# Kernel tuning notes

Measured on AMD Instinct MI355X. Metric: run time of the kernel, lower is better.

The kernel has to match this reference:

```python
import jax, jax.numpy as jnp
import numpy as np

PARENTS = np.array([-1, 0, 1, 1, 1])
NECK_CHAIN = np.array([1, 0])  # neck joint (1) up to root (0)
B, V, F, J, S, E = 512, 5023, 9976, 5, 100, 50
L_STAT, L_DYN, L_FULL, N_BUCKET = 51, 17, 68, 79


def rodrigues(rvec):
    """Axis-angle [N,3] -> rotation matrices [N,3,3]."""
    angle = jnp.linalg.norm(rvec + 1e-8, axis=-1, keepdims=True)  # [N,1]
    axis = rvec / angle
    s = jnp.sin(angle)[..., None]
    c = jnp.cos(angle)[..., None]
    rx, ry, rz = axis[:, 0], axis[:, 1], axis[:, 2]
    z = jnp.zeros_like(rx)
    K = jnp.stack([z, -rz, ry, rz, z, -rx, -ry, rx, z], axis=-1).reshape(-1, 3, 3)
    I = jnp.eye(3, dtype=rvec.dtype)
    return I + s * K + (1.0 - c) * (K @ K)


def verts2lmk(vertices, faces, lmk_faces_idx, lmk_bary):
    lmk_faces = faces[lmk_faces_idx]                               # [B,L,3]
    lmk_verts = jax.vmap(lambda v, f: v[f])(vertices, lmk_faces)   # [B,L,3verts,3xyz]
    return jnp.einsum('blfc,blf->blc', lmk_verts, lmk_bary)


def setup_inputs() -> dict:
    key = jax.random.key(0)
    ks = jax.random.split(key, 16)
    shape_params = jax.random.normal(ks[0], (B, S), jnp.float32)
    expression_params = jax.random.normal(ks[1], (B, E), jnp.float32)
    pose_params = 0.2 * jax.random.normal(ks[2], (B, 6), jnp.float32)
    eye_pose_params = 0.1 * jax.random.normal(ks[3], (B, 6), jnp.float32)
    v_template = jax.random.normal(ks[4], (V, 3), jnp.float32) * 0.1
    shapedirs = jax.random.normal(ks[5], (V, 3, S + E), jnp.float32) * 0.01
    posedirs = jax.random.normal(ks[6], ((J - 1) * 9, V * 3), jnp.float32) * 0.01
    jr = jax.random.uniform(ks[7], (J, V), jnp.float32)
    J_regressor = jr / jnp.sum(jr, axis=1, keepdims=True)
    lbs_weights = jax.nn.softmax(jax.random.normal(ks[8], (V, J), jnp.float32), axis=-1)
    faces = jax.random.randint(ks[9], (F, 3), 0, V)
    lmk_faces_idx = jax.random.randint(ks[10], (L_STAT,), 0, F)
    lb = jax.random.uniform(ks[11], (L_STAT, 3), jnp.float32) + 1e-3
    lmk_bary_coords = lb / jnp.sum(lb, axis=-1, keepdims=True)
    dynamic_lmk_faces_idx = jax.random.randint(ks[12], (N_BUCKET, L_DYN), 0, F)
    db = jax.random.uniform(ks[13], (N_BUCKET, L_DYN, 3), jnp.float32) + 1e-3
    dynamic_lmk_bary_coords = db / jnp.sum(db, axis=-1, keepdims=True)
    full_lmk_faces_idx = jax.random.randint(ks[14], (L_FULL,), 0, F)
    fb = jax.random.uniform(ks[15], (L_FULL, 3), jnp.float32) + 1e-3
    full_lmk_bary_coords = fb / jnp.sum(fb, axis=-1, keepdims=True)
    return {
        'shape_params': shape_params, 'expression_params': expression_params,
        'pose_params': pose_params, 'eye_pose_params': eye_pose_params,
        'v_template': v_template, 'shapedirs': shapedirs, 'posedirs': posedirs,
        'J_regressor': J_regressor, 'lbs_weights': lbs_weights, 'faces': faces,
        'lmk_faces_idx': lmk_faces_idx, 'lmk_bary_coords': lmk_bary_coords,
        'dynamic_lmk_faces_idx': dynamic_lmk_faces_idx,
        'dynamic_lmk_bary_coords': dynamic_lmk_bary_coords,
        'full_lmk_faces_idx': full_lmk_faces_idx,
        'full_lmk_bary_coords': full_lmk_bary_coords,
    }


def reference(shape_params, expression_params, pose_params, eye_pose_params,
              v_template, shapedirs, posedirs, J_regressor, lbs_weights, faces,
              lmk_faces_idx, lmk_bary_coords, dynamic_lmk_faces_idx,
              dynamic_lmk_bary_coords, full_lmk_faces_idx, full_lmk_bary_coords):
    b = shape_params.shape[0]
    nv = v_template.shape[0]
    dt = shape_params.dtype
    betas = jnp.concatenate([shape_params, expression_params], axis=1)          # [B,150]
    neck = jnp.zeros((b, 3), dtype=dt)
    full_pose = jnp.concatenate(
        [pose_params[:, :3], neck, pose_params[:, 3:], eye_pose_params], axis=1)  # [B,15]
    # shape + expression blendshapes
    v_shaped = v_template[None] + jnp.einsum('bl,vcl->bvc', betas, shapedirs)   # [B,V,3]
    joints = jnp.einsum('jv,bvc->bjc', J_regressor, v_shaped)                   # [B,5,3]
    rot_mats = rodrigues(full_pose.reshape(-1, 3)).reshape(b, J, 3, 3)          # [B,5,3,3]
    I3 = jnp.eye(3, dtype=dt)
    pose_feature = (rot_mats[:, 1:] - I3).reshape(b, -1)                        # [B,36]
    v_posed = v_shaped + (pose_feature @ posedirs).reshape(b, nv, 3)
    # kinematic chain -> global joint transforms
    rel_J = joints.at[:, 1:].add(-joints[:, PARENTS[1:]])
    tm = jnp.zeros((b, J, 4, 4), dtype=dt)
    tm = tm.at[:, :, :3, :3].set(rot_mats).at[:, :, :3, 3].set(rel_J).at[:, :, 3, 3].set(1.0)
    chain = [tm[:, 0]]
    for i in range(1, J):
        chain.append(chain[PARENTS[i]] @ tm[:, i])
    A = jnp.stack(chain, axis=1)                                                # [B,5,4,4]
    Rj = jnp.einsum('bjmn,bjn->bjm', A[:, :, :3, :3], joints)
    A_rel = A.at[:, :, :3, 3].add(-Rj)
    # per-vertex skinning
    T = jnp.einsum('vj,bjmn->bvmn', lbs_weights, A_rel)                         # [B,V,4,4]
    vertices = jnp.einsum('bvmn,bvn->bvm', T[:, :, :3, :3], v_posed) + T[:, :, :3, 3]
    # dynamic contour landmark selection from neck kin-chain relative rotation
    aa = full_pose.reshape(b, J, 3)[:, NECK_CHAIN]                              # [B,2,3]
    rc = rodrigues(aa.reshape(-1, 3)).reshape(b, len(NECK_CHAIN), 3, 3)
    rel_rot = jnp.broadcast_to(I3, (b, 3, 3))
    for idx in range(len(NECK_CHAIN)):
        rel_rot = rc[:, idx] @ rel_rot
    sy = jnp.sqrt(rel_rot[:, 0, 0] ** 2 + rel_rot[:, 1, 0] ** 2)
    y_deg = jnp.arctan2(-rel_rot[:, 2, 0], sy) * (180.0 / np.pi)
    y_rot = jnp.round(jnp.minimum(y_deg, 39.0)).astype(jnp.int32)
    neg_mask = y_rot < 0
    big_neg = y_rot < -39
    neg_vals = jnp.where(big_neg, 78, 39 - y_rot)
    y_rot = jnp.where(neg_mask, neg_vals, y_rot)                                # [B] in [0,79)
    dyn_faces = dynamic_lmk_faces_idx[y_rot]                                    # [B,17]
    dyn_bary = dynamic_lmk_bary_coords[y_rot]                                   # [B,17,3]
    lf = jnp.concatenate([dyn_faces, jnp.broadcast_to(lmk_faces_idx[None], (b, lmk_faces_idx.shape[0]))], axis=1)
    lb = jnp.concatenate([dyn_bary, jnp.broadcast_to(lmk_bary_coords[None], (b,) + lmk_bary_coords.shape)], axis=1)
    landmarks2d = verts2lmk(vertices, faces, lf, lb)
    ff = jnp.broadcast_to(full_lmk_faces_idx[None], (b, full_lmk_faces_idx.shape[0]))
    fb = jnp.broadcast_to(full_lmk_bary_coords[None], (b,) + full_lmk_bary_coords.shape)
    landmarks3d = verts2lmk(vertices, faces, ff, fb)
    return (vertices, landmarks2d, landmarks3d)
```

## Files before the change

### kernel.cpp

```cpp
#include <hip/hip_runtime.h>
#include <cstddef>
#include <cstdint>

#define cB   512
#define cV   5023
#define cS   100
#define cE   50
#define cJ   5
#define cLD  17
#define cLF  68

#define cV3    15069
#define cNPAD  15072

#define OUT_V  ((size_t)cB * cV * 3)
#define OUT_L  ((size_t)cB * cLF * 3)

#define WS_BTN    ((size_t)0)
#define WS_ATM    (WS_BTN + (size_t)cNPAD * 96)
#define WS_JS2    (WS_ATM + (size_t)cB * 96)
#define WS_AREL   (WS_JS2 + 2432)
#define WS_YROT   (WS_AREL + (size_t)cB * 60)
#define WS_JSPART (WS_YROT + 512)

typedef __attribute__((ext_vector_type(8))) short short8;
typedef __attribute__((ext_vector_type(4))) float f32x4;

__device__ __forceinline__ unsigned short f2bf(float x) {
  unsigned int u = __float_as_uint(x);
  u = (u + 0x7fffu + ((u >> 16) & 1u)) >> 16;
  return (unsigned short)u;
}

__device__ __forceinline__ void rodrigues9(float rx, float ry, float rz, float* R) {
  float a0 = rx + 1e-8f, a1 = ry + 1e-8f, a2 = rz + 1e-8f;
  float angle = sqrtf(a0 * a0 + a1 * a1 + a2 * a2);
  float inv = 1.0f / angle;
  float x = rx * inv, y = ry * inv, z = rz * inv;
  float s = sinf(angle), c = cosf(angle);
  float t = 1.0f - c;
  float xy = x * y, xz = x * z, yz = y * z;
  R[0] = 1.0f - t * (y * y + z * z);
  R[1] = -s * z + t * xy;
  R[2] =  s * y + t * xz;
  R[3] =  s * z + t * xy;
  R[4] = 1.0f - t * (x * x + z * z);
  R[5] = -s * x + t * yz;
  R[6] = -s * y + t * xz;
  R[7] =  s * x + t * yz;
  R[8] = 1.0f - t * (x * x + y * y);
}

__global__ __launch_bounds__(512) void k_dirs(
    const float* __restrict__ sd, const float* __restrict__ pd,
    const float* __restrict__ jreg, const float* __restrict__ vt,
    unsigned int* __restrict__ btn_u, float* __restrict__ JSpart) {
  __shared__ float sdt[96 * 152];
  __shared__ unsigned short pdt[96 * 38];
  const int t = threadIdx.x;
  const int nb = blockIdx.x;
  const int n0 = nb * 96, v0 = nb * 32;

  const size_t gbase = (size_t)n0 * 150;
  for (int idx = t; idx < 14400; idx += 512) {
    size_t g = gbase + idx;
    float v = (g < (size_t)cV3 * 150) ? sd[g] : 0.f;
    int row = idx / 150, col = idx - row * 150;
    sdt[row * 152 + col] = v;
  }
  for (int e = t; e < 3456; e += 512) {
    int pdk = e / 96, row = e - pdk * 96;
    int n = n0 + row;
    float v = (n < cV3) ? pd[(size_t)pdk * cV3 + n] : 0.f;
    pdt[row * 38 + pdk] = f2bf(v);
  }
  __syncthreads();

#pragma unroll
  for (int it = 0; it < 18; ++it) {
    int e = t + it * 512;
    int row = e / 96, d = e - row * 96;
    unsigned int wv;
    if (d < 75) {
      wv = (unsigned int)f2bf(sdt[row * 152 + 2 * d]) |
           ((unsigned int)f2bf(sdt[row * 152 + 2 * d + 1]) << 16);
    } else if (d < 93) {
      wv = (unsigned int)pdt[row * 38 + (d - 75) * 2] |
           ((unsigned int)pdt[row * 38 + (d - 75) * 2 + 1] << 16);
    } else {
      wv = 0u;
    }
    btn_u[(size_t)(n0 + row) * 96 + d] = wv;
  }

  if (t < 453) {
    int c = t / 151, l = t - c * 151;
    float acc[5] = {0.f, 0.f, 0.f, 0.f, 0.f};
#pragma unroll 8
    for (int v_loc = 0; v_loc < 32; ++v_loc) {
      int v = v0 + v_loc;
      bool ok = (v < cV);
      float x = (l < 150) ? sdt[(v_loc * 3 + c) * 152 + l]
                          : (ok ? vt[v * 3 + c] : 0.f);
#pragma unroll
      for (int j = 0; j < 5; ++j) {
        float g = ok ? jreg[j * cV + v] : 0.f;
        acc[j] = fmaf(g, x, acc[j]);
      }
    }
#pragma unroll
    for (int j = 0; j < 5; ++j)
      JSpart[(size_t)nb * 2272 + (j * 3 + c) * 151 + l] = acc[j];
  }
}

__global__ void k_jsred(const float* __restrict__ JSpart, float* __restrict__ JS2) {
  int e = blockIdx.x * 256 + threadIdx.x;
  if (e >= 2265) return;
  float s = 0.f;
#pragma unroll 8
  for (int p = 0; p < 157; ++p)
    s += JSpart[(size_t)p * 2272 + e];
  int jc = e / 151, l = e - jc * 151;
  JS2[l * 16 + jc] = s;
}

__global__ __launch_bounds__(256) void k_batch(
    const float* __restrict__ shp, const float* __restrict__ expr,
    const float* __restrict__ pose, const float* __restrict__ eyep,
    const float* __restrict__ JS2g, float* __restrict__ Arel,
    int* __restrict__ yrot, unsigned int* __restrict__ atm_u) {
  __shared__ float js2[151 * 16];
  __shared__ float sb[32 * 153];
  __shared__ float pfs[32 * 36];
  const int t = threadIdx.x;
  const int b0 = blockIdx.x * 32;
  for (int i = t; i < 151 * 16; i += 256) js2[i] = JS2g[i];
  for (int e = t; e < 3200; e += 256) {
    int bl = e / 100, l = e - bl * 100;
    sb[bl * 153 + l] = shp[(size_t)(b0 + bl) * 100 + l];
  }
  for (int e = t; e < 1600; e += 256) {
    int bl = e / 50, l = e - bl * 50;
    sb[bl * 153 + 100 + l] = expr[(size_t)(b0 + bl) * 50 + l];
  }
  __syncthreads();

  if (t < 32) {
    int b = b0 + t;
    float jnt[5][3];
    {
      const f32x4* J4 = (const f32x4*)(js2 + 150 * 16);
      f32x4 A = J4[0], Bq = J4[1], Cq = J4[2], Dq = J4[3];
      jnt[0][0] = A.x;  jnt[0][1] = A.y;  jnt[0][2] = A.z;
      jnt[1][0] = A.w;  jnt[1][1] = Bq.x; jnt[1][2] = Bq.y;
      jnt[2][0] = Bq.z; jnt[2][1] = Bq.w; jnt[2][2] = Cq.x;
      jnt[3][0] = Cq.y; jnt[3][1] = Cq.z; jnt[3][2] = Cq.w;
      jnt[4][0] = Dq.x; jnt[4][1] = Dq.y; jnt[4][2] = Dq.z;
    }
    for (int l = 0; l < 150; ++l) {
      const f32x4* J4 = (const f32x4*)(js2 + l * 16);
      f32x4 A = J4[0], Bq = J4[1], Cq = J4[2], Dq = J4[3];
      float beta = sb[t * 153 + l];
      jnt[0][0] = fmaf(beta, A.x,  jnt[0][0]);
      jnt[0][1] = fmaf(beta, A.y,  jnt[0][1]);
      jnt[0][2] = fmaf(beta, A.z,  jnt[0][2]);
      jnt[1][0] = fmaf(beta, A.w,  jnt[1][0]);
      jnt[1][1] = fmaf(beta, Bq.x, jnt[1][1]);
      jnt[1][2] = fmaf(beta, Bq.y, jnt[1][2]);
      jnt[2][0] = fmaf(beta, Bq.z, jnt[2][0]);
      jnt[2][1] = fmaf(beta, Bq.w, jnt[2][1]);
      jnt[2][2] = fmaf(beta, Cq.x, jnt[2][2]);
      jnt[3][0] = fmaf(beta, Cq.y, jnt[3][0]);
      jnt[3][1] = fmaf(beta, Cq.z, jnt[3][1]);
      jnt[3][2] = fmaf(beta, Cq.w, jnt[3][2]);
      jnt[4][0] = fmaf(beta, Dq.x, jnt[4][0]);
      jnt[4][1] = fmaf(beta, Dq.y, jnt[4][1]);
      jnt[4][2] = fmaf(beta, Dq.z, jnt[4][2]);
    }
    float fp[5][3];
    fp[0][0] = pose[b * 6 + 0]; fp[0][1] = pose[b * 6 + 1]; fp[0][2] = pose[b * 6 + 2];
    fp[1][0] = 0.f; fp[1][1] = 0.f; fp[1][2] = 0.f;
    fp[2][0] = pose[b * 6 + 3]; fp[2][1] = pose[b * 6 + 4]; fp[2][2] = pose[b * 6 + 5];
    fp[3][0] = eyep[b * 6 + 0]; fp[3][1] = eyep[b * 6 + 1]; fp[3][2] = eyep[b * 6 + 2];
    fp[4][0] = eyep[b * 6 + 3]; fp[4][1] = eyep[b * 6 + 4]; fp[4][2] = eyep[b * 6 + 5];
    float R[5][9];
#pragma unroll
    for (int j = 0; j < 5; ++j) rodrigues9(fp[j][0], fp[j][1], fp[j][2], R[j]);
#pragma unroll
    for (int j = 1; j < 5; ++j)
#pragma unroll
      for (int r = 0; r < 9; ++r) {
        float id = (r == 0 || r == 4 || r == 8) ? 1.f : 0.f;
        pfs[t * 36 + (j - 1) * 9 + r] = R[j][r] - id;
      }
    float rel[5][3];
#pragma unroll
    for (int c = 0; c < 3; ++c) {
      rel[0][c] = jnt[0][c];
      rel[1][c] = jnt[1][c] - jnt[0][c];
      rel[2][c] = jnt[2][c] - jnt[1][c];
      rel[3][c] = jnt[3][c] - jnt[1][c];
      rel[4][c] = jnt[4][c] - jnt[1][c];
    }
    float GR[5][9], Gt[5][3];
#pragma unroll
    for (int r = 0; r < 9; ++r) GR[0][r] = R[0][r];
#pragma unroll
    for (int c = 0; c < 3; ++c) Gt[0][c] = rel[0][c];
    const int par[5] = {0, 0, 1, 1, 1};
#pragma unroll
    for (int j = 1; j < 5; ++j) {
      int p = par[j];
#pragma unroll
      for (int r = 0; r < 3; ++r) {
#pragma unroll
        for (int cc = 0; cc < 3; ++cc)
          GR[j][r * 3 + cc] = GR[p][r * 3 + 0] * R[j][0 + cc] +
                              GR[p][r * 3 + 1] * R[j][3 + cc] +
                              GR[p][r * 3 + 2] * R[j][6 + cc];
        Gt[j][r] = Gt[p][r] + GR[p][r * 3 + 0] * rel[j][0] +
                              GR[p][r * 3 + 1] * rel[j][1] +
                              GR[p][r * 3 + 2] * rel[j][2];
      }
    }
#pragma unroll
    for (int j = 0; j < 5; ++j)
#pragma unroll
      for (int r = 0; r < 3; ++r) {
        float tj = Gt[j][r] - (GR[j][r * 3 + 0] * jnt[j][0] +
                               GR[j][r * 3 + 1] * jnt[j][1] +
                               GR[j][r * 3 + 2] * jnt[j][2]);
        Arel[b * 60 + j * 12 + r * 4 + 0] = GR[j][r * 3 + 0];
        Arel[b * 60 + j * 12 + r * 4 + 1] = GR[j][r * 3 + 1];
        Arel[b * 60 + j * 12 + r * 4 + 2] = GR[j][r * 3 + 2];
        Arel[b * 60 + j * 12 + r * 4 + 3] = tj;
      }
    float Ra[9], Rb[9];
    rodrigues9(fp[1][0], fp[1][1], fp[1][2], Ra);
    rodrigues9(fp[0][0], fp[0][1], fp[0][2], Rb);
    float r00 = Rb[0] * Ra[0] + Rb[1] * Ra[3] + Rb[2] * Ra[6];
    float r10 = Rb[3] * Ra[0] + Rb[4] * Ra[3] + Rb[5] * Ra[6];
    float r20 = Rb[6] * Ra[0] + Rb[7] * Ra[3] + Rb[8] * Ra[6];
    float sy = sqrtf(r00 * r00 + r10 * r10);
    float ydeg = atan2f(-r20, sy) * 57.29577951308232f;
    int y = (int)rintf(fminf(ydeg, 39.0f));
    if (y < 0) y = (y < -39) ? 78 : (39 - y);
    yrot[b] = y;
  }
  __syncthreads();

#pragma unroll
  for (int it = 0; it < 12; ++it) {
    int e = t + it * 256;
    int bl = e / 96, d = e - bl * 96;
    unsigned int wv;
    if (d < 75) {
      wv = (unsigned int)f2bf(sb[bl * 153 + 2 * d]) |
           ((unsigned int)f2bf(sb[bl * 153 + 2 * d + 1]) << 16);
    } else if (d < 93) {
      wv = (unsigned int)f2bf(pfs[bl * 36 + (d - 75) * 2]) |
           ((unsigned int)f2bf(pfs[bl * 36 + (d - 75) * 2 + 1]) << 16);
    } else {
      wv = 0u;
    }
    atm_u[(size_t)(b0 + bl) * 96 + d] = wv;
  }
}

__global__ __launch_bounds__(256) void k_main(
    const unsigned short* __restrict__ BTn, const unsigned short* __restrict__ ATm,
    const float* __restrict__ Arel, const float* __restrict__ vtempl,
    const float* __restrict__ lbw, float* __restrict__ out) {
  __shared__ __align__(16) unsigned short smem[19200];
  float* Pf = (float*)smem;

  const int bid = blockIdx.x;
  const int r8 = bid & 7, q = bid >> 3;
  const int mb = q & 7, nbh = q >> 3;
  const int nb = (nbh << 3) | r8;
  if (nb >= 157) return;

  const int t = threadIdx.x;
  const int w = t >> 6, L = t & 63;
  const int wm = w >> 1, wn = w & 1;
  const int lr = L & 15, lq = L >> 4;

  const unsigned short* bsrc = BTn + (size_t)nb * 96 * 192;
  uint4 bst[9];
#pragma unroll
  for (int it = 0; it < 9; ++it)
    bst[it] = *(const uint4*)(bsrc + ((size_t)(t + it * 256)) * 8);
#pragma unroll
  for (int it = 0; it < 9; ++it) {
    int e = t + it * 256;
    int row = e / 24, col = e - row * 24;
    *(uint4*)(smem + row * 200 + col * 8) = bst[it];
  }
  __syncthreads();

  f32x4 acc[2][3];
#pragma unroll
  for (int mt = 0; mt < 2; ++mt)
#pragma unroll
    for (int nt = 0; nt < 3; ++nt) acc[mt][nt] = (f32x4){0.f, 0.f, 0.f, 0.f};

  const unsigned short* abase = ATm + ((size_t)mb * 64 + wm * 32 + lr) * 192 + lq * 8;
  short8 af0 = *(const short8*)(abase);
  short8 af1 = *(const short8*)(abase + 16 * 192);
#pragma unroll
  for (int ks = 0; ks < 6; ++ks) {
    short8 nf0, nf1;
    if (ks < 5) {
      nf0 = *(const short8*)(abase + (ks + 1) * 32);
      nf1 = *(const short8*)(abase + 16 * 192 + (ks + 1) * 32);
    }
    const int ko = ks * 32 + lq * 8;
    short8 bf[3];
#pragma unroll
    for (int nt = 0; nt < 3; ++nt)
      bf[nt] = *(const short8*)(smem + (wn * 48 + nt * 16 + lr) * 200 + ko);
#pragma unroll
    for (int nt = 0; nt < 3; ++nt) {
      acc[0][nt] = __builtin_amdgcn_mfma_f32_16x16x32_bf16(af0, bf[nt], acc[0][nt], 0, 0, 0);
      acc[1][nt] = __builtin_amdgcn_mfma_f32_16x16x32_bf16(af1, bf[nt], acc[1][nt], 0, 0, 0);
    }
    af0 = nf0; af1 = nf1;
  }
  __syncthreads();

#pragma unroll
  for (int mt = 0; mt < 2; ++mt)
#pragma unroll
    for (int nt = 0; nt < 3; ++nt) {
      int m_base = wm * 32 + mt * 16 + lq * 4;
      int n_loc  = wn * 48 + nt * 16 + lr;
      *(f32x4*)(Pf + n_loc * 68 + m_base) = acc[mt][nt];
    }
  __syncthreads();

  const int v_loc = t & 31, bgrp = t >> 5;
  const int v = nb * 32 + v_loc;
  float wj[5], vtl[3];
  const bool vok = (v < cV);
#pragma unroll
  for (int j = 0; j < 5; ++j) wj[j] = vok ? lbw[v * 5 + j] : 0.f;
#pragma unroll
  for (int c = 0; c < 3; ++c) vtl[c] = vok ? vtempl[v * 3 + c] : 0.f;

#pragma unroll
  for (int i = 0; i < 8; ++i) {
    const int b_loc = bgrp * 8 + i;
    const float* qb = Arel + ((size_t)mb * 64 + b_loc) * 60;
    float px = Pf[(v_loc * 3 + 0) * 68 + b_loc] + vtl[0];
    float py = Pf[(v_loc * 3 + 1) * 68 + b_loc] + vtl[1];
    float pz = Pf[(v_loc * 3 + 2) * 68 + b_loc] + vtl[2];
    float o0 = 0.f, o1 = 0.f, o2 = 0.f;
#pragma unroll
    for (int j = 0; j < 5; ++j) {
      f32x4 q0 = *(const f32x4*)(qb + j * 12);
      f32x4 q1 = *(const f32x4*)(qb + j * 12 + 4);
      f32x4 q2 = *(const f32x4*)(qb + j * 12 + 8);
      float s0 = q0.x * px + q0.y * py + q0.z * pz + q0.w;
      float s1 = q1.x * px + q1.y * py + q1.z * pz + q1.w;
      float s2 = q2.x * px + q2.y * py + q2.z * pz + q2.w;
      o0 = fmaf(wj[j], s0, o0);
      o1 = fmaf(wj[j], s1, o1);
      o2 = fmaf(wj[j], s2, o2);
    }
    if (vok) {
      const int b = mb * 64 + b_loc;
      size_t off = ((size_t)b * cV + v) * 3;
      out[off + 0] = o0;
      out[off + 1] = o1;
      out[off + 2] = o2;
    }
  }
}

__global__ void k_lmk(const float* __restrict__ verts, const int* __restrict__ faces,
                      const int* __restrict__ lmkf, const float* __restrict__ lmkb,
                      const int* __restrict__ dynf, const float* __restrict__ dynb,
                      const int* __restrict__ fullf, const float* __restrict__ fullb,
                      const int* __restrict__ yrot, float* __restrict__ out) {
  int id = blockIdx.x * 256 + threadIdx.x;
  if (id >= cB * cLF * 2) return;
  int sel = id & 1;
  int r = id >> 1;
  int b = r / cLF, l = r - b * cLF;
  const float* vb = verts + (size_t)b * cV * 3;
  int f; float w0, w1, w2; size_t o;
  if (sel == 0) {
    if (l < cLD) {
      int yb = yrot[b];
      f = dynf[yb * cLD + l];
      const float* bp = dynb + ((size_t)yb * cLD + l) * 3;
      w0 = bp[0]; w1 = bp[1]; w2 = bp[2];
    } else {
      f = lmkf[l - cLD];
      const float* bp = lmkb + (size_t)(l - cLD) * 3;
      w0 = bp[0]; w1 = bp[1]; w2 = bp[2];
    }
    o = OUT_V + ((size_t)b * cLF + l) * 3;
  } else {
    f = fullf[l];
    const float* bp = fullb + (size_t)l * 3;
    w0 = bp[0]; w1 = bp[1]; w2 = bp[2];
    o = OUT_V + OUT_L + ((size_t)b * cLF + l) * 3;
  }
  int i0 = faces[f * 3 + 0] * 3, i1 = faces[f * 3 + 1] * 3, i2 = faces[f * 3 + 2] * 3;
  out[o + 0] = w0 * vb[i0 + 0] + w1 * vb[i1 + 0] + w2 * vb[i2 + 0];
  out[o + 1] = w0 * vb[i0 + 1] + w1 * vb[i1 + 1] + w2 * vb[i2 + 1];
  out[o + 2] = w0 * vb[i0 + 2] + w1 * vb[i1 + 2] + w2 * vb[i2 + 2];
}

extern "C" void kernel_launch(void* const* d_in, const int* in_sizes, int n_in,
                              void* d_out, int out_size, void* d_ws, size_t ws_size,
                              hipStream_t stream) {
  (void)in_sizes; (void)n_in; (void)out_size; (void)ws_size;
  const float* shp  = (const float*)d_in[0];
  const float* expr = (const float*)d_in[1];
  const float* pose = (const float*)d_in[2];
  const float* eyep = (const float*)d_in[3];
  const float* vt   = (const float*)d_in[4];
  const float* sd   = (const float*)d_in[5];
  const float* pd   = (const float*)d_in[6];
  const float* jreg = (const float*)d_in[7];
  const float* lbw  = (const float*)d_in[8];
  const int*   fcs  = (const int*)d_in[9];
  const int*   lmkf = (const int*)d_in[10];
  const float* lmkb = (const float*)d_in[11];
  const int*   dynf = (const int*)d_in[12];
  const float* dynb = (const float*)d_in[13];
  const int*   fullf= (const int*)d_in[14];
  const float* fullb= (const float*)d_in[15];
  float* out = (float*)d_out;
  float* ws  = (float*)d_ws;

  unsigned short* BTn = (unsigned short*)(ws + WS_BTN);
  unsigned short* ATm = (unsigned short*)(ws + WS_ATM);
  float* JS2    = ws + WS_JS2;
  float* Arel   = ws + WS_AREL;
  int*   yrot   = (int*)(ws + WS_YROT);
  float* JSpart = ws + WS_JSPART;

  k_dirs<<<157, 512, 0, stream>>>(sd, pd, jreg, vt, (unsigned int*)BTn, JSpart);
  k_jsred<<<9, 256, 0, stream>>>(JSpart, JS2);
  k_batch<<<16, 256, 0, stream>>>(shp, expr, pose, eyep, JS2, Arel, yrot,
                                  (unsigned int*)ATm);
  k_main<<<1280, 256, 0, stream>>>(BTn, ATm, Arel, vt, lbw, out);
  k_lmk<<<272, 256, 0, stream>>>(out, fcs, lmkf, lmkb, dynf, dynb, fullf, fullb, yrot, out);
}
```

Baseline: 195.1 us.

## Convert shapedirs to bf16 inside main GEMM and split preprocessing across more blocks

Drops the precomputed bf16 B-matrix workspace. The main kernel now reads fp32 shapedirs directly and converts them to bf16 into shared memory, and only a small transposed posedirs bf16 buffer is prebuilt. The joint-regression partial sums are spread over 628 small blocks plus separate posedirs-transpose blocks, and the reduction uses 8 partial groups per element with a shared-memory tree. This removes a 157-block preprocessing pass and the write and re-read of the B workspace. In exchange, each of the 8 batch-tile blocks that share an N tile re-reads fp32 shapedirs and repeats the conversion, which is more global traffic inside k_main.

```diff
diff --git a/kernel.cpp b/kernel.cpp
--- a/kernel.cpp
+++ b/kernel.cpp
@@ -16,11 +16,11 @@
 #define OUT_V  ((size_t)cB * cV * 3)
 #define OUT_L  ((size_t)cB * cLF * 3)
 
-#define WS_BTN    ((size_t)0)
-#define WS_ATM    (WS_BTN + (size_t)cNPAD * 96)
-#define WS_JS2    (WS_ATM + (size_t)cB * 96)
+#define WS_PDT    ((size_t)0)
+#define WS_ATM    (WS_PDT + 271296)
+#define WS_JS2    (WS_ATM + 49152)
 #define WS_AREL   (WS_JS2 + 2432)
-#define WS_YROT   (WS_AREL + (size_t)cB * 60)
+#define WS_YROT   (WS_AREL + 30720)
 #define WS_JSPART (WS_YROT + 512)
 
 typedef __attribute__((ext_vector_type(8))) short short8;
@@ -51,78 +51,79 @@
   R[8] = 1.0f - t * (x * x + y * y);
 }
 
-__global__ __launch_bounds__(512) void k_dirs(
+__global__ __launch_bounds__(512) void k_aux(
     const float* __restrict__ sd, const float* __restrict__ pd,
     const float* __restrict__ jreg, const float* __restrict__ vt,
-    unsigned int* __restrict__ btn_u, float* __restrict__ JSpart) {
-  __shared__ float sdt[96 * 152];
-  __shared__ unsigned short pdt[96 * 38];
+    unsigned int* __restrict__ pdt16_u, float* __restrict__ JSpart) {
+  __shared__ unsigned short T[2304];
   const int t = threadIdx.x;
-  const int nb = blockIdx.x;
-  const int n0 = nb * 96, v0 = nb * 32;
-
-  const size_t gbase = (size_t)n0 * 150;
-  for (int idx = t; idx < 14400; idx += 512) {
-    size_t g = gbase + idx;
-    float v = (g < (size_t)cV3 * 150) ? sd[g] : 0.f;
-    int row = idx / 150, col = idx - row * 150;
-    sdt[row * 152 + col] = v;
-  }
-  for (int e = t; e < 3456; e += 512) {
-    int pdk = e / 96, row = e - pdk * 96;
-    int n = n0 + row;
-    float v = (n < cV3) ? pd[(size_t)pdk * cV3 + n] : 0.f;
-    pdt[row * 38 + pdk] = f2bf(v);
-  }
-  __syncthreads();
-
-#pragma unroll
-  for (int it = 0; it < 18; ++it) {
-    int e = t + it * 512;
-    int row = e / 96, d = e - row * 96;
-    unsigned int wv;
-    if (d < 75) {
-      wv = (unsigned int)f2bf(sdt[row * 152 + 2 * d]) |
-           ((unsigned int)f2bf(sdt[row * 152 + 2 * d + 1]) << 16);
-    } else if (d < 93) {
-      wv = (unsigned int)pdt[row * 38 + (d - 75) * 2] |
-           ((unsigned int)pdt[row * 38 + (d - 75) * 2 + 1] << 16);
-    } else {
-      wv = 0u;
-    }
-    btn_u[(size_t)(n0 + row) * 96 + d] = wv;
-  }
-
-  if (t < 453) {
+  const int bid = blockIdx.x;
+  if (bid < 628) {
+    if (t >= 453) return;
     int c = t / 151, l = t - c * 151;
+    int v0 = bid * 8;
     float acc[5] = {0.f, 0.f, 0.f, 0.f, 0.f};
+#pragma unroll
+    for (int vi = 0; vi < 8; ++vi) {
+      int v = v0 + vi;
+      bool ok = (v < cV);
+      int vc = ok ? v : 0;
+      float x;
+      if (l < 150) x = ok ? sd[(size_t)(v * 3 + c) * 150 + l] : 0.f;
+      else         x = ok ? vt[v * 3 + c] : 0.f;
+#pragma unroll
+      for (int j = 0; j < 5; ++j)
+        acc[j] = fmaf(jreg[j * cV + vc], x, acc[j]);
+    }
+#pragma unroll
+    for (int j = 0; j < 5; ++j)
+      JSpart[(size_t)bid * 2272 + (j * 3 + c) * 151 + l] = acc[j];
+  } else {
+    const int n0 = (bid - 628) * 64;
+    for (int e = t; e < 2304; e += 512) {
+      int kk = e >> 6, ln = e & 63;
+      int n = n0 + ln;
+      float v = (n < cV3) ? pd[(size_t)kk * cV3 + n] : 0.f;
+      T[ln * 36 + kk] = f2bf(v);
+    }
+    __syncthreads();
+    for (int e = t; e < 1152; e += 512) {
+      int ln = e / 18, d = e - ln * 18;
+      int n = n0 + ln;
+      if (n < cNPAD) {
+        unsigned int wv = (unsigned int)T[ln * 36 + 2 * d] |
+                          ((unsigned int)T[ln * 36 + 2 * d + 1] << 16);
+        pdt16_u[(size_t)n * 18 + d] = wv;
+      }
+    }
+  }
+}
+
+__global__ __launch_bounds__(256) void k_jsred(const float* __restrict__ JSpart,
+                                               float* __restrict__ JS2) {
+  __shared__ float red[256];
+  const int t = threadIdx.x;
+  const int e = blockIdx.x * 32 + (t & 31);
+  const int pg = t >> 5;
+  float s = 0.f;
+  if (e < 2265) {
 #pragma unroll 8
-    for (int v_loc = 0; v_loc < 32; ++v_loc) {
-      int v = v0 + v_loc;
-      bool ok = (v < cV);
-      float x = (l < 150) ? sdt[(v_loc * 3 + c) * 152 + l]
-                          : (ok ? vt[v * 3 + c] : 0.f);
-#pragma unroll
-      for (int j = 0; j < 5; ++j) {
-        float g = ok ? jreg[j * cV + v] : 0.f;
-        acc[j] = fmaf(g, x, acc[j]);
-      }
-    }
-#pragma unroll
-    for (int j = 0; j < 5; ++j)
-      JSpart[(size_t)nb * 2272 + (j * 3 + c) * 151 + l] = acc[j];
-  }
-}
-
-__global__ void k_jsred(const float* __restrict__ JSpart, float* __restrict__ JS2) {
-  int e = blockIdx.x * 256 + threadIdx.x;
-  if (e >= 2265) return;
-  float s = 0.f;
-#pragma unroll 8
-  for (int p = 0; p < 157; ++p)
-    s += JSpart[(size_t)p * 2272 + e];
-  int jc = e / 151, l = e - jc * 151;
-  JS2[l * 16 + jc] = s;
+    for (int p = pg; p < 628; p += 8)
+      s += JSpart[(size_t)p * 2272 + e];
+  }
+  red[t] = s;
+  __syncthreads();
+  if (t < 128) red[t] += red[t + 128];
+  __syncthreads();
+  if (t < 64) red[t] += red[t + 64];
+  __syncthreads();
+  if (t < 32) {
+    float v = red[t] + red[t + 32];
+    if (e < 2265) {
+      int jc = e / 151, l = e - jc * 151;
+      JS2[l * 16 + jc] = v;
+    }
+  }
 }
 
 __global__ __launch_bounds__(256) void k_batch(
@@ -269,9 +270,10 @@
 }
 
 __global__ __launch_bounds__(256) void k_main(
-    const unsigned short* __restrict__ BTn, const unsigned short* __restrict__ ATm,
-    const float* __restrict__ Arel, const float* __restrict__ vtempl,
-    const float* __restrict__ lbw, float* __restrict__ out) {
+    const float* __restrict__ sd, const unsigned int* __restrict__ pdt16_u,
+    const unsigned short* __restrict__ ATm, const float* __restrict__ Arel,
+    const float* __restrict__ vtempl, const float* __restrict__ lbw,
+    float* __restrict__ out) {
   __shared__ __align__(16) unsigned short smem[19200];
   float* Pf = (float*)smem;
 
@@ -282,22 +284,50 @@
   if (nb >= 157) return;
 
   const int t = threadIdx.x;
+  const int n0 = nb * 96;
+
+  {
+    const float* sbase = sd + (size_t)n0 * 150;
+    const int vrows = (cV3 - n0 < 96) ? (cV3 - n0) : 96;
+    const int vunits = vrows * 75;
+#pragma unroll
+    for (int it = 0; it < 29; ++it) {
+      int u = t + it * 256;
+      if (u < 7200) {
+        float fx = 0.f, fy = 0.f;
+        if (u < vunits) {
+          float2 f2 = *(const float2*)(sbase + 2 * (size_t)u);
+          fx = f2.x; fy = f2.y;
+        }
+        unsigned int wv = (unsigned int)f2bf(fx) | ((unsigned int)f2bf(fy) << 16);
+        int row = u / 75, cp = u - row * 75;
+        *(unsigned int*)((char*)smem + row * 400 + cp * 4) = wv;
+      }
+    }
+    const unsigned int* pdu = pdt16_u + (size_t)n0 * 18;
+#pragma unroll
+    for (int it = 0; it < 7; ++it) {
+      int u = t + it * 256;
+      if (u < 1728) {
+        unsigned int wv = pdu[u];
+        int row = u / 18, d = u - row * 18;
+        *(unsigned int*)((char*)smem + row * 400 + 300 + d * 4) = wv;
+      }
+    }
+#pragma unroll
+    for (int it = 0; it < 3; ++it) {
+      int u = t + it * 256;
+      if (u < 672) {
+        int row = u / 7, d = u - row * 7;
+        *(unsigned int*)((char*)smem + row * 400 + 372 + d * 4) = 0u;
+      }
+    }
+  }
+  __syncthreads();
+
   const int w = t >> 6, L = t & 63;
   const int wm = w >> 1, wn = w & 1;
   const int lr = L & 15, lq = L >> 4;
-
-  const unsigned short* bsrc = BTn + (size_t)nb * 96 * 192;
-  uint4 bst[9];
-#pragma unroll
-  for (int it = 0; it < 9; ++it)
-    bst[it] = *(const uint4*)(bsrc + ((size_t)(t + it * 256)) * 8);
-#pragma unroll
-  for (int it = 0; it < 9; ++it) {
-    int e = t + it * 256;
-    int row = e / 24, col = e - row * 24;
-    *(uint4*)(smem + row * 200 + col * 8) = bst[it];
-  }
-  __syncthreads();
 
   f32x4 acc[2][3];
 #pragma unroll
@@ -437,17 +467,17 @@
   float* out = (float*)d_out;
   float* ws  = (float*)d_ws;
 
-  unsigned short* BTn = (unsigned short*)(ws + WS_BTN);
-  unsigned short* ATm = (unsigned short*)(ws + WS_ATM);
+  unsigned int*   pdt16 = (unsigned int*)(ws + WS_PDT);
+  unsigned short* ATm   = (unsigned short*)(ws + WS_ATM);
   float* JS2    = ws + WS_JS2;
   float* Arel   = ws + WS_AREL;
   int*   yrot   = (int*)(ws + WS_YROT);
   float* JSpart = ws + WS_JSPART;
 
-  k_dirs<<<157, 512, 0, stream>>>(sd, pd, jreg, vt, (unsigned int*)BTn, JSpart);
-  k_jsred<<<9, 256, 0, stream>>>(JSpart, JS2);
+  k_aux<<<864, 512, 0, stream>>>(sd, pd, jreg, vt, pdt16, JSpart);
+  k_jsred<<<71, 256, 0, stream>>>(JSpart, JS2);
   k_batch<<<16, 256, 0, stream>>>(shp, expr, pose, eyep, JS2, Arel, yrot,
                                   (unsigned int*)ATm);
-  k_main<<<1280, 256, 0, stream>>>(BTn, ATm, Arel, vt, lbw, out);
+  k_main<<<1280, 256, 0, stream>>>(sd, pdt16, ATm, Arel, vt, lbw, out);
   k_lmk<<<272, 256, 0, stream>>>(out, fcs, lmkf, lmkb, dynf, dynb, fullf, fullb, yrot, out);
 }
```

After: 185.7 us. 4.8% less time.
